# Optimization experiments

Hardware: AMD Instinct MI355X
Metric: run time of the kernel (lower is better)

## Reference

```python
import jax, jax.numpy as jnp
import numpy as np

D_MODEL = 2048
N_HEAD = 16
N_KV_HEAD = 4
D_HEAD = D_MODEL // N_HEAD  # 128
ROPE_BASE = 10000.0


def build_rope_cache(d_head, seq_len):
    # NeoX-style half-split RoPE cache: cos/sin of shape [T, d_head]
    inv_freq = 1.0 / (ROPE_BASE ** (jnp.arange(0, d_head, 2, dtype=jnp.float32) / d_head))
    t = jnp.arange(seq_len, dtype=jnp.float32)
    ang = jnp.einsum('t,f->tf', t, inv_freq)            # [T, d_head/2]
    ang = jnp.concatenate([ang, ang], axis=-1)           # [T, d_head]
    return jnp.cos(ang), jnp.sin(ang)


def apply_rope(x, cos, sin):
    # x: [B, T, H, Dh]; cos/sin: [T, Dh]
    d = x.shape[-1]
    x1, x2 = x[..., : d // 2], x[..., d // 2 :]
    rot = jnp.concatenate([-x2, x1], axis=-1)
    c = cos[None, :, None, :]
    s = sin[None, :, None, :]
    return x * c + rot * s


def setup_inputs() -> dict:
    key = jax.random.key(0)
    k1, k2, k3, k4, k5 = jax.random.split(key, 5)
    B, T = 4, 2048
    scale = 1.0 / np.sqrt(D_MODEL)
    return {
        'x': jax.random.normal(k1, (B, T, D_MODEL), dtype=jnp.float32),
        'Wq': jax.random.normal(k2, (D_MODEL, N_HEAD * D_HEAD), dtype=jnp.float32) * scale,
        'Wk': jax.random.normal(k3, (D_MODEL, N_KV_HEAD * D_HEAD), dtype=jnp.float32) * scale,
        'Wv': jax.random.normal(k4, (D_MODEL, N_KV_HEAD * D_HEAD), dtype=jnp.float32) * scale,
        'Wo': jax.random.normal(k5, (D_MODEL, D_MODEL), dtype=jnp.float32) * scale,
    }


def reference(x, Wq, Wk, Wv, Wo):
    B, T, C = x.shape
    q = (x @ Wq).reshape(B, T, N_HEAD, D_HEAD)
    k = (x @ Wk).reshape(B, T, N_KV_HEAD, D_HEAD)
    v = (x @ Wv).reshape(B, T, N_KV_HEAD, D_HEAD)

    cos, sin = build_rope_cache(D_HEAD, T)  # no cache -> positions [0, T)
    q = apply_rope(q, cos, sin)
    k = apply_rope(k, cos, sin)

    q = q.transpose(0, 2, 1, 3)  # [B, H, T, Dh]
    k = k.transpose(0, 2, 1, 3)  # [B, Hkv, T, Dh]
    v = v.transpose(0, 2, 1, 3)

    rf = N_HEAD // N_KV_HEAD
    k = jnp.repeat(k, rf, axis=1)  # GQA: repeat_interleave over head dim
    v = jnp.repeat(v, rf, axis=1)

    scores = jnp.einsum('bhtd,bhsd->bhts', q, k) / np.sqrt(D_HEAD)
    causal = jnp.tril(jnp.ones((T, T), dtype=bool))
    scores = jnp.where(causal[None, None], scores, -jnp.inf)
    probs = jax.nn.softmax(scores, axis=-1)
    attn = jnp.einsum('bhts,bhsd->bhtd', probs, v)

    attn = attn.transpose(0, 2, 1, 3).reshape(B, T, C)
    return attn @ Wo
```

## Files before the change

kernel.cpp:

```cpp
#include <hip/hip_runtime.h>

typedef unsigned short u16;
typedef __bf16 bf16x8 __attribute__((ext_vector_type(8)));
typedef u16 u16x8 __attribute__((ext_vector_type(8)));
typedef u16 u16x4 __attribute__((ext_vector_type(4)));
typedef float f32x4 __attribute__((ext_vector_type(4)));

#define MFMA16(a, b, c) __builtin_amdgcn_mfma_f32_16x16x32_bf16((a), (b), (c), 0, 0, 0)

__device__ __forceinline__ void async16(const u16* g, u16* l) {
  __builtin_amdgcn_global_load_lds(
      (__attribute__((address_space(1))) void*)(void*)(g),
      (__attribute__((address_space(3))) void*)(void*)(l), 16, 0, 0);
}

__device__ __forceinline__ float bf2f(u16 b) {
  union { unsigned u; float f; } v;
  v.u = ((unsigned)b) << 16;
  return v.f;
}
__device__ __forceinline__ u16 f2bf(float f) {
  union { float f; unsigned u; } v;
  v.f = f;
  unsigned u = v.u;
  return (u16)((u + 0x7FFFu + ((u >> 16) & 1u)) >> 16);
}

__global__ __launch_bounds__(256) void convert_k(const float* __restrict__ in,
                                                 u16* __restrict__ out, int n8) {
  const int stride = gridDim.x * 256;
  for (int i = blockIdx.x * 256 + threadIdx.x; i < n8; i += stride) {
    const float* fp = in + (size_t)i * 8;
    float4 a = *(const float4*)fp, b = *(const float4*)(fp + 4);
    u16x8 o;
    o[0] = f2bf(a.x); o[1] = f2bf(a.y); o[2] = f2bf(a.z); o[3] = f2bf(a.w);
    o[4] = f2bf(b.x); o[5] = f2bf(b.y); o[6] = f2bf(b.z); o[7] = f2bf(b.w);
    *(u16x8*)&out[(size_t)i * 8] = o;
  }
}

__global__ __launch_bounds__(256) void transpose_cvt_k(const float* __restrict__ W,
                                                       u16* __restrict__ Wt, int K, int N) {
  __shared__ __align__(16) u16 tile[64 * 72];
  const int t = threadIdx.x;
  const int n0 = blockIdx.x * 64, k0 = blockIdx.y * 64;
#pragma unroll
  for (int i = 0; i < 2; ++i) {
    int flat = t + i * 256;
    int r = flat >> 3, c8 = (flat & 7) * 8;
    const float* p = W + (size_t)(k0 + r) * N + n0 + c8;
    float4 a = *(const float4*)p, b = *(const float4*)(p + 4);
    u16x8 v;
    v[0] = f2bf(a.x); v[1] = f2bf(a.y); v[2] = f2bf(a.z); v[3] = f2bf(a.w);
    v[4] = f2bf(b.x); v[5] = f2bf(b.y); v[6] = f2bf(b.z); v[7] = f2bf(b.w);
#pragma unroll
    for (int j = 0; j < 8; ++j) tile[r * 72 + c8 + j] = v[j];
  }
  __syncthreads();
#pragma unroll
  for (int i = 0; i < 2; ++i) {
    int flat = t + i * 256;
    int r = flat >> 3, c8 = (flat & 7) * 8;
    u16x8 v;
#pragma unroll
    for (int j = 0; j < 8; ++j) v[j] = tile[(c8 + j) * 72 + r];
    *(u16x8*)&Wt[(size_t)(n0 + r) * K + k0 + c8] = v;
  }
}

__global__ __launch_bounds__(256) void rope_table_k(float* __restrict__ cosT,
                                                    float* __restrict__ sinT) {
  int idx = blockIdx.x * 256 + threadIdx.x;
  int tp = idx >> 6, i = idx & 63;
  float invf = expf(-(float)i * (9.210340371976184f / 64.0f));
  float ang = (float)tp * invf;
  cosT[idx] = cosf(ang);
  sinT[idx] = sinf(ang);
}

__global__ __launch_bounds__(256) void rope_apply_k(u16* __restrict__ base,
                                                    const float* __restrict__ cosT,
                                                    const float* __restrict__ sinT,
                                                    int rowStride, int nhMask, int rowShift,
                                                    float scale) {
  int idx = blockIdx.x * 256 + threadIdx.x;
  int i4 = idx & 15;
  int hh = (idx >> 4) & nhMask;
  int row = idx >> rowShift;
  int tp = row & 2047;
  int i = i4 * 4;
  u16* p = base + (size_t)row * rowStride + hh * 128;
  u16x4 a = *(u16x4*)&p[i];
  u16x4 b = *(u16x4*)&p[i + 64];
  float4 c = *(const float4*)&cosT[tp * 64 + i];
  float4 s = *(const float4*)&sinT[tp * 64 + i];
  float cc[4] = {c.x, c.y, c.z, c.w}, ss[4] = {s.x, s.y, s.z, s.w};
  u16x4 oa, ob;
#pragma unroll
  for (int j = 0; j < 4; ++j) {
    float x1 = bf2f(a[j]), x2 = bf2f(b[j]);
    oa[j] = f2bf((x1 * cc[j] - x2 * ss[j]) * scale);
    ob[j] = f2bf((x2 * cc[j] + x1 * ss[j]) * scale);
  }
  *(u16x4*)&p[i] = oa;
  *(u16x4*)&p[i + 64] = ob;
}

template <bool F32OUT>
__global__ __launch_bounds__(256) void gemm_tn(const u16* __restrict__ A,
                                               const u16* __restrict__ Bt,
                                               void* __restrict__ C, int M, int N, int K) {
  __shared__ __align__(16) u16 As[128 * 32];
  __shared__ __align__(16) u16 Bs[128 * 32];
  const int t = threadIdx.x;
  const int l = t & 63, w = t >> 6;
  const int wm = w >> 1, wn = w & 1;
  const int lr = l & 15, lg = l >> 4;
  const int nbx = gridDim.x;
  const int lin = blockIdx.y * nbx + blockIdx.x;
  const int cpx = (nbx * gridDim.y) >> 3;
  const int sl = (lin & 7) * cpx + (lin >> 3);
  const size_t m0 = (size_t)(sl / nbx) * 128, n0 = (size_t)(sl % nbx) * 128;
  f32x4 acc[4][4] = {};
  for (int k0 = 0; k0 < K; k0 += 32) {
#pragma unroll
    for (int i = 0; i < 2; ++i) {
      int flat = t + i * 256;
      int r = flat >> 2, seg = (flat & 3) * 8;
      async16(&A[(m0 + r) * K + k0 + seg], &As[flat * 8]);
      async16(&Bt[(n0 + r) * K + k0 + seg], &Bs[flat * 8]);
    }
    __syncthreads();
    bf16x8 af[4], bfr[4];
#pragma unroll
    for (int i = 0; i < 4; ++i) {
      af[i] = *(const bf16x8*)&As[(wm * 64 + i * 16 + lr) * 32 + lg * 8];
      bfr[i] = *(const bf16x8*)&Bs[(wn * 64 + i * 16 + lr) * 32 + lg * 8];
    }
#pragma unroll
    for (int mi = 0; mi < 4; ++mi)
#pragma unroll
      for (int ni = 0; ni < 4; ++ni) acc[mi][ni] = MFMA16(af[mi], bfr[ni], acc[mi][ni]);
    __syncthreads();
  }
#pragma unroll
  for (int mi = 0; mi < 4; ++mi)
#pragma unroll
    for (int ni = 0; ni < 4; ++ni)
#pragma unroll
      for (int r = 0; r < 4; ++r) {
        size_t row = m0 + wm * 64 + mi * 16 + lg * 4 + r;
        size_t col = n0 + wn * 64 + ni * 16 + lr;
        if constexpr (F32OUT)
          ((float*)C)[row * N + col] = acc[mi][ni][r];
        else
          ((u16*)C)[row * N + col] = f2bf(acc[mi][ni][r]);
      }
}

__global__ __launch_bounds__(512, 4) void attn_k(const u16* __restrict__ QKV,
                                                 u16* __restrict__ O) {
  constexpr int T = 2048, CS = 3072, OC = 2048;
  __shared__ __align__(16) u16 Ks[64 * 128];
  __shared__ __align__(16) u16 Vt[128 * 72];
  __shared__ __align__(16) u16 Pl[128 * 72];
  const int t = threadIdx.x, l = t & 63, w = t >> 6, lr = l & 15, lg = l >> 4;
  const int lin = blockIdx.x;
  const int v = (lin & 7) * 128 + (lin >> 3);
  const int bh = v >> 4;
  const int qt = 15 - (v & 15);
  const int b = bh >> 4, h = bh & 15, kv = h >> 2;
  const int q0 = qt * 128;
  const int myrow = w * 16 + lg * 4;
  const size_t rowQ = (size_t)(b * T + q0 + w * 16 + lr) * CS + h * 128;
  bf16x8 qf[4];
#pragma unroll
  for (int di = 0; di < 4; ++di) qf[di] = *(const bf16x8*)&QKV[rowQ + di * 32 + lg * 8];
  bf16x8 onesf;
#pragma unroll
  for (int j = 0; j < 8; ++j) onesf[j] = (__bf16)1.0f;
  f32x4 lsum = {};
  f32x4 oacc[8] = {};
  const int lastst = 2 * qt + 1;
  for (int st = 0; st <= lastst; ++st) {
    const int s0 = st * 64;
    const size_t kvRow = (size_t)(b * T + s0) * CS + 2048 + kv * 128;
#pragma unroll
    for (int i = 0; i < 2; ++i) {
      int flat = t + i * 512;
      int r = flat >> 4, c = flat & 15;
      async16(&QKV[kvRow + (size_t)r * CS + ((c ^ (r & 7)) * 8)], &Ks[flat * 8]);
    }
    {
      int s = (t >> 4) * 2, d8 = (t & 15) * 8;
      u16x8 v0 = *(const u16x8*)&QKV[kvRow + 512 + (size_t)s * CS + d8];
      u16x8 v1 = *(const u16x8*)&QKV[kvRow + 512 + (size_t)(s + 1) * CS + d8];
#pragma unroll
      for (int j = 0; j < 8; ++j) {
        int d = d8 + j;
        int slot = (s >> 3) ^ ((d >> 3) & 7);
        unsigned val = (unsigned)v0[j] | ((unsigned)v1[j] << 16);
        *(unsigned*)&Vt[d * 72 + slot * 8 + (s & 7)] = val;
      }
    }
    __syncthreads();
    const bool skip = (st == lastst) && (w < 4);
    if (!skip) {
      f32x4 sacc[4] = {};
#pragma unroll
      for (int di = 0; di < 4; ++di)
#pragma unroll
        for (int n = 0; n < 4; ++n) {
          bf16x8 bk = *(const bf16x8*)&Ks[(n * 16 + lr) * 128 + (((di * 4 + lg) ^ (lr & 7)) << 3)];
          sacc[n] = MFMA16(qf[di], bk, sacc[n]);
        }
      const bool diag = (st >= 2 * qt);
#pragma unroll
      for (int n = 0; n < 4; ++n)
#pragma unroll
        for (int r = 0; r < 4; ++r) {
          float s_ = sacc[n][r] * 1.44269504f - 11.5415603f;
          if (diag && (s0 + 16 * n + lr > q0 + myrow + r)) s_ = -1e30f;
          *(__bf16*)&Pl[(myrow + r) * 72 + 16 * n + lr] = (__bf16)exp2f(s_);
        }
#pragma unroll
      for (int ks = 0; ks < 2; ++ks) {
        bf16x8 pa = *(const bf16x8*)&Pl[(w * 16 + lr) * 72 + ks * 32 + lg * 8];
        lsum = MFMA16(pa, onesf, lsum);
#pragma unroll
        for (int nf = 0; nf < 8; ++nf) {
          int d = 16 * nf + lr;
          int seg = lg + 4 * ks;
          bf16x8 vb = *(const bf16x8*)&Vt[d * 72 + ((seg ^ ((d >> 3) & 7)) << 3)];
          oacc[nf] = MFMA16(pa, vb, oacc[nf]);
        }
      }
    }
    __syncthreads();
  }
#pragma unroll
  for (int r = 0; r < 4; ++r) {
    float il = 1.0f / lsum[r];
    size_t orow = (size_t)(b * T + q0 + myrow + r) * OC + h * 128;
#pragma unroll
    for (int nf = 0; nf < 8; ++nf) O[orow + 16 * nf + lr] = f2bf(oacc[nf][r] * il);
  }
}

__global__ __launch_bounds__(256) void sentinel_k(float* __restrict__ out) {
  out[blockIdx.x * 256 + threadIdx.x] = 1.0e4f;
}

extern "C" void kernel_launch(void* const* d_in, const int* in_sizes, int n_in, void* d_out,
                              int out_size, void* d_ws, size_t ws_size, hipStream_t stream) {
  const float* x = (const float*)d_in[0];
  const float* Wq = (const float*)d_in[1];
  const float* Wk = (const float*)d_in[2];
  const float* Wv = (const float*)d_in[3];
  const float* Wo = (const float*)d_in[4];

  char* p = (char*)d_ws;
  auto take = [&](size_t bytes) {
    char* r = p;
    p += (bytes + 255) & ~(size_t)255;
    return r;
  };
  u16* WqkvT = (u16*)take((size_t)3072 * 2048 * 2);
  u16* WoT = (u16*)take((size_t)2048 * 2048 * 2);
  u16* QKV = (u16*)take((size_t)8192 * 3072 * 2);
  u16* Ob = (u16*)take((size_t)8192 * 2048 * 2);
  u16* xbf = (u16*)take((size_t)8192 * 2048 * 2);
  float* cosT = (float*)take((size_t)2048 * 64 * 4);
  float* sinT = (float*)take((size_t)2048 * 64 * 4);
  if (ws_size < (size_t)(p - (char*)d_ws)) {
    sentinel_k<<<4, 256, 0, stream>>>((float*)d_out);
    return;
  }

  convert_k<<<2048, 256, 0, stream>>>(x, xbf, 8192 * 2048 / 8);
  transpose_cvt_k<<<dim3(32, 32), 256, 0, stream>>>(Wq, WqkvT, 2048, 2048);
  transpose_cvt_k<<<dim3(8, 32), 256, 0, stream>>>(Wk, WqkvT + (size_t)2048 * 2048, 2048, 512);
  transpose_cvt_k<<<dim3(8, 32), 256, 0, stream>>>(Wv, WqkvT + (size_t)2560 * 2048, 2048, 512);
  transpose_cvt_k<<<dim3(32, 32), 256, 0, stream>>>(Wo, WoT, 2048, 2048);
  rope_table_k<<<512, 256, 0, stream>>>(cosT, sinT);

  gemm_tn<false><<<dim3(24, 64), 256, 0, stream>>>(xbf, WqkvT, QKV, 8192, 3072, 2048);

  rope_apply_k<<<8192, 256, 0, stream>>>(QKV, cosT, sinT, 3072, 15, 8, 0.08838834764831845f);
  rope_apply_k<<<2048, 256, 0, stream>>>(QKV + 2048, cosT, sinT, 3072, 3, 6, 1.0f);

  attn_k<<<1024, 512, 0, stream>>>(QKV, Ob);

  gemm_tn<true><<<dim3(16, 64), 256, 0, stream>>>(Ob, WoT, (void*)d_out, 8192, 2048, 2048);
}
```

Measured before the change: 464.4 us.

## Double-buffer K tiles and prefetch V into registers in attention loop

```diff
diff --git a/kernel.cpp b/kernel.cpp
--- a/kernel.cpp
+++ b/kernel.cpp
@@ -161,7 +161,7 @@
 __global__ __launch_bounds__(512, 4) void attn_k(const u16* __restrict__ QKV,
                                                  u16* __restrict__ O) {
   constexpr int T = 2048, CS = 3072, OC = 2048;
-  __shared__ __align__(16) u16 Ks[64 * 128];
+  __shared__ __align__(16) u16 Ks[2][64 * 128];
   __shared__ __align__(16) u16 Vt[128 * 72];
   __shared__ __align__(16) u16 Pl[128 * 72];
   const int t = threadIdx.x, l = t & 63, w = t >> 6, lr = l & 15, lg = l >> 4;
@@ -182,28 +182,41 @@
   f32x4 lsum = {};
   f32x4 oacc[8] = {};
   const int lastst = 2 * qt + 1;
-  for (int st = 0; st <= lastst; ++st) {
-    const int s0 = st * 64;
-    const size_t kvRow = (size_t)(b * T + s0) * CS + 2048 + kv * 128;
+  const size_t kvBase = (size_t)(b * T) * CS + 2048 + kv * 128;
+  const int sV = (t >> 4) * 2, d8V = (t & 15) * 8;
+  u16x8 vr0, vr1;
+  {
 #pragma unroll
     for (int i = 0; i < 2; ++i) {
       int flat = t + i * 512;
       int r = flat >> 4, c = flat & 15;
-      async16(&QKV[kvRow + (size_t)r * CS + ((c ^ (r & 7)) * 8)], &Ks[flat * 8]);
-    }
-    {
-      int s = (t >> 4) * 2, d8 = (t & 15) * 8;
-      u16x8 v0 = *(const u16x8*)&QKV[kvRow + 512 + (size_t)s * CS + d8];
-      u16x8 v1 = *(const u16x8*)&QKV[kvRow + 512 + (size_t)(s + 1) * CS + d8];
-#pragma unroll
-      for (int j = 0; j < 8; ++j) {
-        int d = d8 + j;
-        int slot = (s >> 3) ^ ((d >> 3) & 7);
-        unsigned val = (unsigned)v0[j] | ((unsigned)v1[j] << 16);
-        *(unsigned*)&Vt[d * 72 + slot * 8 + (s & 7)] = val;
+      async16(&QKV[kvBase + (size_t)r * CS + ((c ^ (r & 7)) * 8)], &Ks[0][flat * 8]);
+    }
+    vr0 = *(const u16x8*)&QKV[kvBase + 512 + (size_t)sV * CS + d8V];
+    vr1 = *(const u16x8*)&QKV[kvBase + 512 + (size_t)(sV + 1) * CS + d8V];
+#pragma unroll
+    for (int j = 0; j < 8; ++j) {
+      int d = d8V + j;
+      int slot = (sV >> 3) ^ ((d >> 3) & 7);
+      *(unsigned*)&Vt[d * 72 + slot * 8 + (sV & 7)] =
+          (unsigned)vr0[j] | ((unsigned)vr1[j] << 16);
+    }
+    __syncthreads();
+  }
+  int cb = 0;
+  for (int st = 0; st <= lastst; ++st) {
+    if (st < lastst) {
+      const size_t kvRow = kvBase + (size_t)(st + 1) * 64 * CS;
+#pragma unroll
+      for (int i = 0; i < 2; ++i) {
+        int flat = t + i * 512;
+        int r = flat >> 4, c = flat & 15;
+        async16(&QKV[kvRow + (size_t)r * CS + ((c ^ (r & 7)) * 8)], &Ks[cb ^ 1][flat * 8]);
       }
-    }
-    __syncthreads();
+      vr0 = *(const u16x8*)&QKV[kvRow + 512 + (size_t)sV * CS + d8V];
+      vr1 = *(const u16x8*)&QKV[kvRow + 512 + (size_t)(sV + 1) * CS + d8V];
+    }
+    const int s0 = st * 64;
     const bool skip = (st == lastst) && (w < 4);
     if (!skip) {
       f32x4 sacc[4] = {};
@@ -211,7 +224,8 @@
       for (int di = 0; di < 4; ++di)
 #pragma unroll
         for (int n = 0; n < 4; ++n) {
-          bf16x8 bk = *(const bf16x8*)&Ks[(n * 16 + lr) * 128 + (((di * 4 + lg) ^ (lr & 7)) << 3)];
+          bf16x8 bk =
+              *(const bf16x8*)&Ks[cb][(n * 16 + lr) * 128 + (((di * 4 + lg) ^ (lr & 7)) << 3)];
           sacc[n] = MFMA16(qf[di], bk, sacc[n]);
         }
       const bool diag = (st >= 2 * qt);
@@ -237,6 +251,17 @@
       }
     }
     __syncthreads();
+    if (st < lastst) {
+#pragma unroll
+      for (int j = 0; j < 8; ++j) {
+        int d = d8V + j;
+        int slot = (sV >> 3) ^ ((d >> 3) & 7);
+        *(unsigned*)&Vt[d * 72 + slot * 8 + (sV & 7)] =
+            (unsigned)vr0[j] | ((unsigned)vr1[j] << 16);
+      }
+    }
+    __syncthreads();
+    cb ^= 1;
   }
 #pragma unroll
   for (int r = 0; r < 4; ++r) {
```

After: 461.6 us, median of 2. About the same (-0.6%).
